# Performance work log

Measured on AMD Instinct MI355X. Metric: run time of the kernel, lower is better.

## Reference

```python
import jax, jax.numpy as jnp
import numpy as np

B, T, E, H = 2, 2048, 1024, 16
HS = E // H  # head_size = 64
EPS = 1e-5


def _layernorm(x, g, b):
    mu = jnp.mean(x, axis=-1, keepdims=True)
    var = jnp.mean(jnp.square(x - mu), axis=-1, keepdims=True)
    return (x - mu) * jax.lax.rsqrt(var + EPS) * g + b


def _block_forward(x, wq, wk, wv, wp, bp, ln1_g, ln1_b, ln2_g, ln2_b,
                   w1, b1, w2, b2, w3, b3, wg_att, bg_att, wg_ff, bg_ff):
    Bc, Tc, Ec = x.shape
    # --- multi-head causal self-attention on ln1(x) ---
    h = _layernorm(x, ln1_g, ln1_b)
    q = jnp.einsum('bte,hek->bhtk', h, wq)  # [B,H,T,HS]
    k = jnp.einsum('bte,hek->bhtk', h, wk)
    v = jnp.einsum('bte,hek->bhtk', h, wv)
    scores = jnp.einsum('bhtk,bhsk->bhts', q, k) * (HS ** -0.5)
    causal = jnp.tril(jnp.ones((Tc, Tc), dtype=bool))
    scores = jnp.where(causal, scores, jnp.finfo(scores.dtype).min)
    wei = jax.nn.softmax(scores, axis=-1)  # [B,H,T,T] (returned, as in torch)
    attn = jnp.einsum('bhts,bhsk->bhtk', wei, v)
    # concat heads in head order -> [B,T,H*HS]
    attn = attn.transpose(0, 2, 1, 3).reshape(Bc, Tc, H * HS)
    sa_out = attn @ wp + bp
    # gated residual: gate from new value, multiply residual (old x)
    gate = jax.nn.sigmoid(sa_out @ wg_att + bg_att)
    x = sa_out + gate * x
    # --- feed-forward on ln2(x) ---
    h2 = _layernorm(x, ln2_g, ln2_b)
    f = jax.nn.gelu(h2 @ w1 + b1, approximate=False)   # [B,T,4E]
    f = jax.nn.gelu(f @ w2 + b2, approximate=False)    # [B,T,2E]
    f = f @ w3 + b3                                     # [B,T,E]
    gate2 = jax.nn.sigmoid(f @ wg_ff + bg_ff)
    x = f + gate2 * x
    return x, wei


def setup_inputs() -> dict:
    key = jax.random.key(0)
    ks = jax.random.split(key, 24)
    s = 0.02
    n = lambda i, shape: (jax.random.normal(ks[i], shape) * s).astype(jnp.float32)
    return {
        'x': jax.random.normal(ks[0], (B, T, E), dtype=jnp.float32),
        'wq': n(1, (H, E, HS)), 'wk': n(2, (H, E, HS)), 'wv': n(3, (H, E, HS)),
        'wp': n(4, (H * HS, E)), 'bp': jnp.zeros((E,), jnp.float32),
        'ln1_g': jnp.ones((E,), jnp.float32), 'ln1_b': jnp.zeros((E,), jnp.float32),
        'ln2_g': jnp.ones((E,), jnp.float32), 'ln2_b': jnp.zeros((E,), jnp.float32),
        'w1': n(5, (E, 4 * E)), 'b1': jnp.zeros((4 * E,), jnp.float32),
        'w2': n(6, (4 * E, 2 * E)), 'b2': jnp.zeros((2 * E,), jnp.float32),
        'w3': n(7, (2 * E, E)), 'b3': jnp.zeros((E,), jnp.float32),
        'wg_att': n(8, (E, E)), 'bg_att': jnp.zeros((E,), jnp.float32),
        'wg_ff': n(9, (E, E)), 'bg_ff': jnp.zeros((E,), jnp.float32),
    }


def reference(x, wq, wk, wv, wp, bp, ln1_g, ln1_b, ln2_g, ln2_b,
              w1, b1, w2, b2, w3, b3, wg_att, bg_att, wg_ff, bg_ff):
    return _block_forward(x, wq, wk, wv, wp, bp, ln1_g, ln1_b, ln2_g, ln2_b,
                          w1, b1, w2, b2, w3, b3, wg_att, bg_att, wg_ff, bg_ff)
```

## Files before the change

### kernel.cpp

```cpp
#include <hip/hip_runtime.h>
#include <hip/hip_bf16.h>

typedef unsigned short u16;
typedef __attribute__((ext_vector_type(8))) short short8;
typedef __attribute__((ext_vector_type(4))) float floatx4;

#define DI __device__ __forceinline__

constexpr int Tn  = 2048;
constexpr int En  = 1024;
constexpr int BTn = 4096;

DI float bf2f(u16 u) { union { unsigned int i; float f; } v; v.i = (unsigned int)u << 16; return v.f; }
DI u16 f2bf(float f) {
  union { float f; unsigned int i; } u; u.f = f;
  unsigned int r = u.i + 0x7FFFu + ((u.i >> 16) & 1u);
  return (u16)(r >> 16);
}
DI float gelu_f(float x) { return 0.5f * x * (1.f + erff(x * 0.70710678118654752f)); }
DI float sigmoid_f(float x) { return 1.f / (1.f + __expf(-x)); }

DI void gload_lds16(const u16* g, u16* l) {
  __builtin_amdgcn_global_load_lds(
      (const __attribute__((address_space(1))) unsigned int*)g,
      (__attribute__((address_space(3))) unsigned int*)l, 16, 0, 0);
}

template <int EPI>
__launch_bounds__(256, 2)
__global__ void gemm_bt(const u16* __restrict__ A, const u16* __restrict__ Bt,
                        const float* __restrict__ bias, u16* __restrict__ C,
                        int M, int N, int K) {
  __shared__ __align__(16) u16 As[3][128 * 32];
  __shared__ __align__(16) u16 Bs[3][128 * 32];
  const int tid = threadIdx.x;
  const int m0 = blockIdx.y << 7, n0 = blockIdx.x << 7;
  const int lane = tid & 63, l15 = lane & 15, quad = lane >> 4;
  const int wave = tid >> 6;
  const int wm = (wave >> 1) << 6, wn = (wave & 1) << 6;

  const int ra = tid >> 2, c8 = (tid & 3) << 3;
  const u16* pa0 = A + (size_t)(m0 + ra) * K + c8;
  const u16* pa1 = pa0 + (size_t)64 * K;
  const u16* pb0 = Bt + (size_t)(n0 + ra) * K + c8;
  const u16* pb1 = pb0 + (size_t)64 * K;
  const int lo = ra * 32 + c8;

  auto STG = [&](int b, int kt) {
    const int ko = kt << 5;
    gload_lds16(pa0 + ko, &As[b][lo]);
    gload_lds16(pa1 + ko, &As[b][lo + 64 * 32]);
    gload_lds16(pb0 + ko, &Bs[b][lo]);
    gload_lds16(pb1 + ko, &Bs[b][lo + 64 * 32]);
  };

  const int nk = K >> 5;
  STG(0, 0); STG(1, 1); STG(2, 2);

  floatx4 acc[4][4] = {};
  int cur = 0;
  for (int k = 0; k < nk; ++k) {
    const int rem = nk - k;
    if (rem > 2)       asm volatile("s_waitcnt vmcnt(8)" ::: "memory");
    else if (rem == 2) asm volatile("s_waitcnt vmcnt(4)" ::: "memory");
    else               asm volatile("s_waitcnt vmcnt(0)" ::: "memory");
    __builtin_amdgcn_s_barrier();
    __builtin_amdgcn_sched_barrier(0);
    const u16* Ab = As[cur];
    const u16* Bb = Bs[cur];
    short8 af[4], bfr[4];
#pragma unroll
    for (int i = 0; i < 4; ++i) {
      af[i]  = *(const short8*)&Ab[(wm + i * 16 + l15) * 32 + quad * 8];
      bfr[i] = *(const short8*)&Bb[(wn + i * 16 + l15) * 32 + quad * 8];
    }
#pragma unroll
    for (int i = 0; i < 4; ++i)
#pragma unroll
      for (int j = 0; j < 4; ++j)
        acc[i][j] = __builtin_amdgcn_mfma_f32_16x16x32_bf16(af[i], bfr[j], acc[i][j], 0, 0, 0);
    __builtin_amdgcn_s_barrier();
    __builtin_amdgcn_sched_barrier(0);
    if (k + 3 < nk) STG(cur, k + 3);
    cur = (cur == 2) ? 0 : cur + 1;
  }
#pragma unroll
  for (int j = 0; j < 4; ++j) {
    const int col = n0 + wn + j * 16 + l15;
    const float bv = bias ? bias[col] : 0.f;
#pragma unroll
    for (int i = 0; i < 4; ++i) {
#pragma unroll
      for (int r = 0; r < 4; ++r) {
        const int row = m0 + wm + i * 16 + quad * 4 + r;
        float v = acc[i][j][r] + bv;
        if (EPI == 1) v = gelu_f(v);
        if (EPI == 2) v = sigmoid_f(v);
        C[(size_t)row * N + col] = f2bf(v);
      }
    }
  }
}

__launch_bounds__(256, 2)
__global__ void attn_scores(const u16* __restrict__ qkv, float* __restrict__ wei,
                            float* __restrict__ lsum) {
  const int bh = blockIdx.z, b = bh >> 4, h = bh & 15;
  const int m0 = blockIdx.y << 7, n0 = blockIdx.x << 7;
  float* weib = wei + (size_t)bh * Tn * Tn;
  const int tid = threadIdx.x;
  if (n0 > m0 + 127) {
    const float4 z = {0.f, 0.f, 0.f, 0.f};
#pragma unroll
    for (int it = 0; it < 16; ++it) {
      int lin = it * 256 + tid;
      int r = lin >> 5, c4 = (lin & 31) << 2;
      *(float4*)&weib[(size_t)(m0 + r) * Tn + n0 + c4] = z;
    }
    return;
  }
  __shared__ __align__(16) u16 Qs[128 * 64];
  __shared__ __align__(16) u16 Ks[128 * 64];
  const int lane = tid & 63, l15 = lane & 15, quad = lane >> 4;
  const int wave = tid >> 6;
  const int wm = (wave >> 1) << 6, wn = (wave & 1) << 6;
  const u16* qb = qkv + (size_t)b * Tn * 3072 + h * 64;
  const u16* kb = qb + 1024;
#pragma unroll
  for (int it = 0; it < 4; ++it) {
    int lin = it * 256 + tid;
    int r = lin >> 3, cc = (lin & 7) << 3;
    gload_lds16(&qb[(size_t)(m0 + r) * 3072 + cc], &Qs[r * 64 + cc]);
    gload_lds16(&kb[(size_t)(n0 + r) * 3072 + cc], &Ks[r * 64 + cc]);
  }
  __syncthreads();
  floatx4 acc[4][4] = {};
#pragma unroll
  for (int ks = 0; ks < 2; ++ks) {
    short8 af[4], bfr[4];
#pragma unroll
    for (int i = 0; i < 4; ++i) {
      af[i]  = *(const short8*)&Qs[(wm + i * 16 + l15) * 64 + ks * 32 + quad * 8];
      bfr[i] = *(const short8*)&Ks[(wn + i * 16 + l15) * 64 + ks * 32 + quad * 8];
    }
#pragma unroll
    for (int i = 0; i < 4; ++i)
#pragma unroll
      for (int j = 0; j < 4; ++j)
        acc[i][j] = __builtin_amdgcn_mfma_f32_16x16x32_bf16(af[i], bfr[j], acc[i][j], 0, 0, 0);
  }
#pragma unroll
  for (int i = 0; i < 4; ++i) {
#pragma unroll
    for (int r = 0; r < 4; ++r) {
      const int row = m0 + wm + i * 16 + quad * 4 + r;
      float ps = 0.f;
#pragma unroll
      for (int j = 0; j < 4; ++j) {
        const int col = n0 + wn + j * 16 + l15;
        float p = (col <= row) ? __expf(acc[i][j][r] * 0.125f) : 0.f;
        weib[(size_t)row * Tn + col] = p;
        ps += p;
      }
      float v = ps;
      v += __shfl_xor(v, 1); v += __shfl_xor(v, 2);
      v += __shfl_xor(v, 4); v += __shfl_xor(v, 8);
      if (l15 == 0) atomicAdd(&lsum[bh * Tn + row], v);
    }
  }
}

__launch_bounds__(256, 2)
__global__ void attn_pv(float* __restrict__ wei, const u16* __restrict__ vT,
                        const float* __restrict__ lsum, u16* __restrict__ attn_out) {
  const int bh = blockIdx.z, b = bh >> 4, h = bh & 15;
  const int m0 = blockIdx.x << 7;
  float* weib = wei + (size_t)bh * Tn * Tn;
  const u16* vtb = vT + (size_t)bh * 64 * Tn;
  __shared__ __align__(16) u16 Ps[128 * 32];
  __shared__ __align__(16) u16 Vs[64 * 32];
  const int tid = threadIdx.x;
  const int lane = tid & 63, l15 = lane & 15, quad = lane >> 4;
  const int wave = tid >> 6;
  const int ra = tid >> 2, c8 = (tid & 3) << 3;
  const float inv0 = 1.f / lsum[bh * Tn + m0 + ra];
  const float inv1 = 1.f / lsum[bh * Tn + m0 + ra + 64];
  floatx4 acc[2][4] = {};
  const int kmax = m0 + 128;
  for (int k0 = 0; k0 < kmax; k0 += 32) {
    gload_lds16(&vtb[(size_t)ra * Tn + k0 + c8], &Vs[ra * 32 + c8]);
#pragma unroll
    for (int half = 0; half < 2; ++half) {
      const int r = ra + half * 64;
      const float inv = half ? inv1 : inv0;
      size_t go = (size_t)(m0 + r) * Tn + k0 + c8;
      float4 a = *(float4*)&weib[go];
      float4 b4 = *(float4*)&weib[go + 4];
      a.x *= inv; a.y *= inv; a.z *= inv; a.w *= inv;
      b4.x *= inv; b4.y *= inv; b4.z *= inv; b4.w *= inv;
      u16 o8[8] = { f2bf(a.x), f2bf(a.y), f2bf(a.z), f2bf(a.w),
                    f2bf(b4.x), f2bf(b4.y), f2bf(b4.z), f2bf(b4.w) };
      *(uint4*)&Ps[r * 32 + c8] = *(uint4*)o8;
      *(float4*)&weib[go] = a;
      *(float4*)&weib[go + 4] = b4;
    }
    __syncthreads();
    short8 af[2], bfr[4];
#pragma unroll
    for (int i = 0; i < 2; ++i)
      af[i] = *(const short8*)&Ps[(wave * 32 + i * 16 + l15) * 32 + quad * 8];
#pragma unroll
    for (int j = 0; j < 4; ++j)
      bfr[j] = *(const short8*)&Vs[(j * 16 + l15) * 32 + quad * 8];
#pragma unroll
    for (int i = 0; i < 2; ++i)
#pragma unroll
      for (int j = 0; j < 4; ++j)
        acc[i][j] = __builtin_amdgcn_mfma_f32_16x16x32_bf16(af[i], bfr[j], acc[i][j], 0, 0, 0);
    __syncthreads();
  }
#pragma unroll
  for (int i = 0; i < 2; ++i)
#pragma unroll
    for (int j = 0; j < 4; ++j)
#pragma unroll
      for (int r = 0; r < 4; ++r) {
        const int row = m0 + wave * 32 + i * 16 + quad * 4 + r;
        const int col = j * 16 + l15;
        attn_out[(size_t)(b * Tn + row) * En + h * 64 + col] = f2bf(acc[i][j][r]);
      }
}

__global__ void transpose_wf(const float* __restrict__ in, u16* __restrict__ out, int R, int Cc) {
  __shared__ u16 t[64][65];
  const int tid = threadIdx.x;
  const int r0 = blockIdx.y << 6, c0 = blockIdx.x << 6;
#pragma unroll
  for (int it = 0; it < 4; ++it) {
    int lin = it * 256 + tid;
    int r = lin >> 4, c4 = (lin & 15) << 2;
    float4 v = *(const float4*)&in[(size_t)(r0 + r) * Cc + c0 + c4];
    t[r][c4 + 0] = f2bf(v.x); t[r][c4 + 1] = f2bf(v.y);
    t[r][c4 + 2] = f2bf(v.z); t[r][c4 + 3] = f2bf(v.w);
  }
  __syncthreads();
#pragma unroll
  for (int it = 0; it < 2; ++it) {
    int lin = it * 256 + tid;
    int r = lin >> 3, cc = (lin & 7) << 3;
    u16 t8[8];
#pragma unroll
    for (int e = 0; e < 8; ++e) t8[e] = t[cc + e][r];
    *(uint4*)&out[(size_t)(c0 + r) * R + r0 + cc] = *(uint4*)t8;
  }
}

__global__ void repack_qkvw(const float* __restrict__ wq, const float* __restrict__ wk,
                            const float* __restrict__ wv, u16* __restrict__ out) {
  const int which = blockIdx.z;
  const float* w = which == 0 ? wq : (which == 1 ? wk : wv);
  const int h = blockIdx.y;
  const int e0 = blockIdx.x << 6;
  __shared__ u16 t[64][65];
  const int tid = threadIdx.x;
  const float* ib = w + (size_t)h * 1024 * 64;
#pragma unroll
  for (int it = 0; it < 4; ++it) {
    int lin = it * 256 + tid;
    int r = lin >> 4, c4 = (lin & 15) << 2;
    float4 v = *(const float4*)&ib[(size_t)(e0 + r) * 64 + c4];
    t[r][c4 + 0] = f2bf(v.x); t[r][c4 + 1] = f2bf(v.y);
    t[r][c4 + 2] = f2bf(v.z); t[r][c4 + 3] = f2bf(v.w);
  }
  __syncthreads();
  u16* ob = out + ((size_t)which * 1024 + h * 64) * 1024;
#pragma unroll
  for (int it = 0; it < 2; ++it) {
    int lin = it * 256 + tid;
    int r = lin >> 3, cc = (lin & 7) << 3;
    u16 t8[8];
#pragma unroll
    for (int e = 0; e < 8; ++e) t8[e] = t[cc + e][r];
    *(uint4*)&ob[(size_t)r * 1024 + e0 + cc] = *(uint4*)t8;
  }
}

__global__ void transpose_v(const u16* __restrict__ qkv, u16* __restrict__ vT) {
  const int bh = blockIdx.z, b = bh >> 4, h = bh & 15;
  const int s0 = blockIdx.x << 6;
  __shared__ u16 t[64][65];
  const int tid = threadIdx.x;
  const u16* ib = qkv + (size_t)b * Tn * 3072 + 2048 + h * 64;
#pragma unroll
  for (int it = 0; it < 2; ++it) {
    int lin = it * 256 + tid;
    int r = lin >> 3, cc = (lin & 7) << 3;
    uint4 v = *(const uint4*)&ib[(size_t)(s0 + r) * 3072 + cc];
    u16 t8[8]; *(uint4*)t8 = v;
#pragma unroll
    for (int e = 0; e < 8; ++e) t[r][cc + e] = t8[e];
  }
  __syncthreads();
  u16* ob = vT + (size_t)bh * 64 * Tn;
#pragma unroll
  for (int it = 0; it < 2; ++it) {
    int lin = it * 256 + tid;
    int r = lin >> 3, cc = (lin & 7) << 3;
    u16 t8[8];
#pragma unroll
    for (int e = 0; e < 8; ++e) t8[e] = t[cc + e][r];
    *(uint4*)&ob[(size_t)r * Tn + s0 + cc] = *(uint4*)t8;
  }
}

__launch_bounds__(256)
__global__ void layernorm_k(const float* __restrict__ x, const float* __restrict__ g,
                            const float* __restrict__ be, u16* __restrict__ out) {
  const int row = blockIdx.x;
  const int tid = threadIdx.x;
  const float* xr = x + (size_t)row * En;
  float4 xv = *(const float4*)&xr[tid * 4];
  float s = xv.x + xv.y + xv.z + xv.w;
  float sq = xv.x * xv.x + xv.y * xv.y + xv.z * xv.z + xv.w * xv.w;
#pragma unroll
  for (int o = 1; o < 64; o <<= 1) { s += __shfl_xor(s, o); sq += __shfl_xor(sq, o); }
  __shared__ float red[8];
  const int wave = tid >> 6, lane = tid & 63;
  if (lane == 0) { red[wave] = s; red[wave + 4] = sq; }
  __syncthreads();
  const float S  = red[0] + red[1] + red[2] + red[3];
  const float SQ = red[4] + red[5] + red[6] + red[7];
  const float mu = S * (1.f / 1024.f);
  const float var = SQ * (1.f / 1024.f) - mu * mu;
  const float rstd = rsqrtf(var + 1e-5f);
  float4 gv = *(const float4*)&g[tid * 4];
  float4 bv = *(const float4*)&be[tid * 4];
  ushort4 ov;
  ov.x = f2bf((xv.x - mu) * rstd * gv.x + bv.x);
  ov.y = f2bf((xv.y - mu) * rstd * gv.y + bv.y);
  ov.z = f2bf((xv.z - mu) * rstd * gv.z + bv.z);
  ov.w = f2bf((xv.w - mu) * rstd * gv.w + bv.w);
  *(ushort4*)&out[(size_t)row * En + tid * 4] = ov;
}

__global__ void gated_residual(const u16* __restrict__ val, const u16* __restrict__ gate,
                               const float* __restrict__ res, float* __restrict__ out) {
  const size_t i = ((size_t)blockIdx.x * 256 + threadIdx.x) * 4;
  ushort4 v = *(const ushort4*)&val[i];
  ushort4 g = *(const ushort4*)&gate[i];
  float4 r = *(const float4*)&res[i];
  float4 o;
  o.x = bf2f(v.x) + bf2f(g.x) * r.x;
  o.y = bf2f(v.y) + bf2f(g.y) * r.y;
  o.z = bf2f(v.z) + bf2f(g.z) * r.z;
  o.w = bf2f(v.w) + bf2f(g.w) * r.w;
  *(float4*)&out[i] = o;
}

extern "C" void kernel_launch(void* const* d_in, const int* in_sizes, int n_in,
                              void* d_out, int out_size, void* d_ws, size_t ws_size,
                              hipStream_t stream) {
  const float* x    = (const float*)d_in[0];
  const float* wq   = (const float*)d_in[1];
  const float* wk   = (const float*)d_in[2];
  const float* wv   = (const float*)d_in[3];
  const float* wp   = (const float*)d_in[4];
  const float* bp   = (const float*)d_in[5];
  const float* ln1g = (const float*)d_in[6];
  const float* ln1b = (const float*)d_in[7];
  const float* ln2g = (const float*)d_in[8];
  const float* ln2b = (const float*)d_in[9];
  const float* w1   = (const float*)d_in[10];
  const float* b1   = (const float*)d_in[11];
  const float* w2   = (const float*)d_in[12];
  const float* b2   = (const float*)d_in[13];
  const float* w3   = (const float*)d_in[14];
  const float* b3   = (const float*)d_in[15];
  const float* wga  = (const float*)d_in[16];
  const float* bga  = (const float*)d_in[17];
  const float* wgf  = (const float*)d_in[18];
  const float* bgf  = (const float*)d_in[19];

  float* out_x = (float*)d_out;
  float* wei   = out_x + (size_t)BTn * En;

  char* wsb = (char*)d_ws;
  size_t off = 0;
  auto alloc = [&](size_t bytes) { char* p = wsb + off; off += (bytes + 255) & ~(size_t)255; return p; };
  float* lsum = (float*)alloc((size_t)32 * Tn * 4);
  u16* WqkvT = (u16*)alloc((size_t)3072 * 1024 * 2);
  u16* wpT   = (u16*)alloc((size_t)1024 * 1024 * 2);
  u16* wgaT  = (u16*)alloc((size_t)1024 * 1024 * 2);
  u16* w1T   = (u16*)alloc((size_t)4096 * 1024 * 2);
  u16* w2T   = (u16*)alloc((size_t)2048 * 4096 * 2);
  u16* w3T   = (u16*)alloc((size_t)1024 * 2048 * 2);
  u16* wgfT  = (u16*)alloc((size_t)1024 * 1024 * 2);
  u16* h1    = (u16*)alloc((size_t)BTn * En * 2);
  u16* qkv   = (u16*)alloc((size_t)BTn * 3072 * 2);
  u16* vT    = (u16*)alloc((size_t)32 * 64 * Tn * 2);
  u16* attn  = (u16*)alloc((size_t)BTn * En * 2);
  u16* sa    = (u16*)alloc((size_t)BTn * En * 2);
  u16* glin  = (u16*)alloc((size_t)BTn * En * 2);
  float* x1  = (float*)alloc((size_t)BTn * En * 4);
  u16* h2 = h1;
  u16* f1 = qkv;
  u16* f2 = attn;
  u16* f3 = glin;
  u16* g2 = h1;

  hipMemsetAsync(lsum, 0, (size_t)32 * Tn * 4, stream);
  repack_qkvw<<<dim3(16, 16, 3), 256, 0, stream>>>(wq, wk, wv, WqkvT);
  transpose_wf<<<dim3(16, 16), 256, 0, stream>>>(wp,  wpT,  1024, 1024);
  transpose_wf<<<dim3(16, 16), 256, 0, stream>>>(wga, wgaT, 1024, 1024);
  transpose_wf<<<dim3(64, 16), 256, 0, stream>>>(w1,  w1T,  1024, 4096);
  transpose_wf<<<dim3(32, 64), 256, 0, stream>>>(w2,  w2T,  4096, 2048);
  transpose_wf<<<dim3(16, 32), 256, 0, stream>>>(w3,  w3T,  2048, 1024);
  transpose_wf<<<dim3(16, 16), 256, 0, stream>>>(wgf, wgfT, 1024, 1024);

  layernorm_k<<<BTn, 256, 0, stream>>>(x, ln1g, ln1b, h1);
  gemm_bt<0><<<dim3(24, 32), 256, 0, stream>>>(h1, WqkvT, nullptr, qkv, BTn, 3072, 1024);
  transpose_v<<<dim3(32, 1, 32), 256, 0, stream>>>(qkv, vT);
  attn_scores<<<dim3(16, 16, 32), 256, 0, stream>>>(qkv, wei, lsum);
  attn_pv<<<dim3(16, 1, 32), 256, 0, stream>>>(wei, vT, lsum, attn);
  gemm_bt<0><<<dim3(8, 32), 256, 0, stream>>>(attn, wpT, bp, sa, BTn, 1024, 1024);
  gemm_bt<2><<<dim3(8, 32), 256, 0, stream>>>(sa, wgaT, bga, glin, BTn, 1024, 1024);
  gated_residual<<<BTn, 256, 0, stream>>>(sa, glin, x, x1);
  layernorm_k<<<BTn, 256, 0, stream>>>(x1, ln2g, ln2b, h2);
  gemm_bt<1><<<dim3(32, 32), 256, 0, stream>>>(h2, w1T, b1, f1, BTn, 4096, 1024);
  gemm_bt<1><<<dim3(16, 32), 256, 0, stream>>>(f1, w2T, b2, f2, BTn, 2048, 4096);
  gemm_bt<0><<<dim3(8, 32), 256, 0, stream>>>(f2, w3T, b3, f3, BTn, 1024, 2048);
  gemm_bt<2><<<dim3(8, 32), 256, 0, stream>>>(f3, wgfT, bgf, g2, BTn, 1024, 1024);
  gated_residual<<<BTn, 256, 0, stream>>>(f3, g2, x1, out_x);
}
```

Baseline: 1.304 ms.

## Fuse attention probs and PV into one kernel, recompute QK instead of rereading wei

The scores kernel now only computes row sums of exp(scores), plus zero-fills the upper triangle; it no longer writes the lower triangle of wei. A new fused kernel recomputes QK^T per tile, normalizes by the row sum, writes the final fp32 probabilities once and feeds bf16 P into the PV MFMA. K and V tiles are double-buffered in swizzled LDS, and row tiles are ordered to balance causal work. This removes one fp32 write plus a read-modify-write of the large wei tensor, at the cost of computing QK^T twice and a more complex pipeline.

```diff
diff --git a/kernel.cpp b/kernel.cpp
--- a/kernel.cpp
+++ b/kernel.cpp
@@ -103,7 +103,7 @@
 }
 
 __launch_bounds__(256, 2)
-__global__ void attn_scores(const u16* __restrict__ qkv, float* __restrict__ wei,
+__global__ void attn_rowsum(const u16* __restrict__ qkv, float* __restrict__ wei,
                             float* __restrict__ lsum) {
   const int bh = blockIdx.z, b = bh >> 4, h = bh & 15;
   const int m0 = blockIdx.y << 7, n0 = blockIdx.x << 7;
@@ -130,8 +130,9 @@
   for (int it = 0; it < 4; ++it) {
     int lin = it * 256 + tid;
     int r = lin >> 3, cc = (lin & 7) << 3;
-    gload_lds16(&qb[(size_t)(m0 + r) * 3072 + cc], &Qs[r * 64 + cc]);
-    gload_lds16(&kb[(size_t)(n0 + r) * 3072 + cc], &Ks[r * 64 + cc]);
+    int cs = cc ^ ((r & 7) << 3);
+    gload_lds16(&qb[(size_t)(m0 + r) * 3072 + cs], &Qs[r * 64 + cc]);
+    gload_lds16(&kb[(size_t)(n0 + r) * 3072 + cs], &Ks[r * 64 + cc]);
   }
   __syncthreads();
   floatx4 acc[4][4] = {};
@@ -140,8 +141,10 @@
     short8 af[4], bfr[4];
 #pragma unroll
     for (int i = 0; i < 4; ++i) {
-      af[i]  = *(const short8*)&Qs[(wm + i * 16 + l15) * 64 + ks * 32 + quad * 8];
-      bfr[i] = *(const short8*)&Ks[(wn + i * 16 + l15) * 64 + ks * 32 + quad * 8];
+      const int qr = wm + i * 16 + l15;
+      const int kr = wn + i * 16 + l15;
+      af[i]  = *(const short8*)&Qs[qr * 64 + ((ks * 32 + quad * 8) ^ ((qr & 7) << 3))];
+      bfr[i] = *(const short8*)&Ks[kr * 64 + ((ks * 32 + quad * 8) ^ ((kr & 7) << 3))];
     }
 #pragma unroll
     for (int i = 0; i < 4; ++i)
@@ -159,7 +162,6 @@
       for (int j = 0; j < 4; ++j) {
         const int col = n0 + wn + j * 16 + l15;
         float p = (col <= row) ? __expf(acc[i][j][r] * 0.125f) : 0.f;
-        weib[(size_t)row * Tn + col] = p;
         ps += p;
       }
       float v = ps;
@@ -170,64 +172,149 @@
   }
 }
 
-__launch_bounds__(256, 2)
-__global__ void attn_pv(float* __restrict__ wei, const u16* __restrict__ vT,
-                        const float* __restrict__ lsum, u16* __restrict__ attn_out) {
+__launch_bounds__(512, 2)
+__global__ void attn_fused(const u16* __restrict__ qkv, const u16* __restrict__ vT,
+                           const float* __restrict__ lsum, float* __restrict__ wei,
+                           u16* __restrict__ attn_out) {
   const int bh = blockIdx.z, b = bh >> 4, h = bh & 15;
-  const int m0 = blockIdx.x << 7;
+  const int xm = blockIdx.x;
+  const int mt = (xm & 1) ? (15 - (xm >> 1)) : (xm >> 1);
+  const int m0 = mt << 7;
   float* weib = wei + (size_t)bh * Tn * Tn;
+  const u16* qb = qkv + (size_t)b * Tn * 3072 + h * 64;
+  const u16* kb = qb + 1024;
   const u16* vtb = vT + (size_t)bh * 64 * Tn;
-  __shared__ __align__(16) u16 Ps[128 * 32];
-  __shared__ __align__(16) u16 Vs[64 * 32];
+
+  __shared__ __align__(16) u16 Ks[2][128 * 64];
+  __shared__ __align__(16) u16 Vs[2][64 * 128];
+  __shared__ __align__(16) u16 Ps[128 * 128];
+
   const int tid = threadIdx.x;
   const int lane = tid & 63, l15 = lane & 15, quad = lane >> 4;
-  const int wave = tid >> 6;
-  const int ra = tid >> 2, c8 = (tid & 3) << 3;
-  const float inv0 = 1.f / lsum[bh * Tn + m0 + ra];
-  const float inv1 = 1.f / lsum[bh * Tn + m0 + ra + 64];
-  floatx4 acc[2][4] = {};
-  const int kmax = m0 + 128;
-  for (int k0 = 0; k0 < kmax; k0 += 32) {
-    gload_lds16(&vtb[(size_t)ra * Tn + k0 + c8], &Vs[ra * 32 + c8]);
-#pragma unroll
-    for (int half = 0; half < 2; ++half) {
-      const int r = ra + half * 64;
-      const float inv = half ? inv1 : inv0;
-      size_t go = (size_t)(m0 + r) * Tn + k0 + c8;
-      float4 a = *(float4*)&weib[go];
-      float4 b4 = *(float4*)&weib[go + 4];
-      a.x *= inv; a.y *= inv; a.z *= inv; a.w *= inv;
-      b4.x *= inv; b4.y *= inv; b4.z *= inv; b4.w *= inv;
-      u16 o8[8] = { f2bf(a.x), f2bf(a.y), f2bf(a.z), f2bf(a.w),
-                    f2bf(b4.x), f2bf(b4.y), f2bf(b4.z), f2bf(b4.w) };
-      *(uint4*)&Ps[r * 32 + c8] = *(uint4*)o8;
-      *(float4*)&weib[go] = a;
-      *(float4*)&weib[go + 4] = b4;
-    }
-    __syncthreads();
-    short8 af[2], bfr[4];
-#pragma unroll
-    for (int i = 0; i < 2; ++i)
-      af[i] = *(const short8*)&Ps[(wave * 32 + i * 16 + l15) * 32 + quad * 8];
-#pragma unroll
-    for (int j = 0; j < 4; ++j)
-      bfr[j] = *(const short8*)&Vs[(j * 16 + l15) * 32 + quad * 8];
-#pragma unroll
-    for (int i = 0; i < 2; ++i)
-#pragma unroll
-      for (int j = 0; j < 4; ++j)
-        acc[i][j] = __builtin_amdgcn_mfma_f32_16x16x32_bf16(af[i], bfr[j], acc[i][j], 0, 0, 0);
-    __syncthreads();
-  }
-#pragma unroll
-  for (int i = 0; i < 2; ++i)
-#pragma unroll
-    for (int j = 0; j < 4; ++j)
+  const int w = tid >> 6;
+  const int rm = w >> 2, cn = w & 3;
+  const int pm = w >> 1, pc = w & 1;
+
+  const int rk = tid >> 3, ck = (tid & 7) << 3;
+  const int rv = tid >> 4, cv = (tid & 15) << 3;
+  const int cks = ck ^ ((rk & 7) << 3);
+  const int cvs = cv ^ ((rv & 7) << 3);
+
+  auto STAGE = [&](int buf, int nt) {
+    const int n0 = nt << 7;
+    gload_lds16(&kb[(size_t)(n0 + rk) * 3072 + cks], &Ks[buf][rk * 64 + ck]);
+    gload_lds16(&kb[(size_t)(n0 + 64 + rk) * 3072 + cks], &Ks[buf][(64 + rk) * 64 + ck]);
+    gload_lds16(&vtb[(size_t)rv * Tn + n0 + cvs], &Vs[buf][rv * 128 + cv]);
+    gload_lds16(&vtb[(size_t)(32 + rv) * Tn + n0 + cvs], &Vs[buf][(32 + rv) * 128 + cv]);
+  };
+
+  gload_lds16(&qb[(size_t)(m0 + rk) * 3072 + cks], &Ps[rk * 64 + ck]);
+  gload_lds16(&qb[(size_t)(m0 + 64 + rk) * 3072 + cks], &Ps[(64 + rk) * 64 + ck]);
+  STAGE(0, 0);
+  if (mt >= 1) {
+    STAGE(1, 1);
+    asm volatile("s_waitcnt vmcnt(8)" ::: "memory");
+  } else {
+    asm volatile("s_waitcnt vmcnt(4)" ::: "memory");
+  }
+  __builtin_amdgcn_s_barrier();
+  __builtin_amdgcn_sched_barrier(0);
+
+  short8 af[4][2];
+#pragma unroll
+  for (int i = 0; i < 4; ++i)
+#pragma unroll
+    for (int ks = 0; ks < 2; ++ks) {
+      const int qr = rm * 64 + i * 16 + l15;
+      af[i][ks] = *(const short8*)&Ps[qr * 64 + ((ks * 32 + quad * 8) ^ ((qr & 7) << 3))];
+    }
+  asm volatile("s_waitcnt lgkmcnt(0)" ::: "memory");
+  __builtin_amdgcn_sched_barrier(0);
+  __builtin_amdgcn_s_barrier();
+  __builtin_amdgcn_sched_barrier(0);
+
+  float inv[4][4];
+#pragma unroll
+  for (int i = 0; i < 4; ++i)
+#pragma unroll
+    for (int r = 0; r < 4; ++r)
+      inv[i][r] = 1.f / lsum[bh * Tn + m0 + rm * 64 + i * 16 + quad * 4 + r];
+
+  floatx4 acc_o[2][2] = {};
+  for (int nt = 0; nt <= mt; ++nt) {
+    const int cbuf = nt & 1;
+    if (nt < mt) asm volatile("s_waitcnt vmcnt(4)" ::: "memory");
+    else         asm volatile("s_waitcnt vmcnt(0)" ::: "memory");
+    __builtin_amdgcn_s_barrier();
+    __builtin_amdgcn_sched_barrier(0);
+
+    floatx4 acc_s[4][2] = {};
+#pragma unroll
+    for (int ks = 0; ks < 2; ++ks) {
+      short8 bk[2];
+#pragma unroll
+      for (int j = 0; j < 2; ++j) {
+        const int kr = cn * 32 + j * 16 + l15;
+        bk[j] = *(const short8*)&Ks[cbuf][kr * 64 + ((ks * 32 + quad * 8) ^ ((kr & 7) << 3))];
+      }
+#pragma unroll
+      for (int i = 0; i < 4; ++i)
+#pragma unroll
+        for (int j = 0; j < 2; ++j)
+          acc_s[i][j] = __builtin_amdgcn_mfma_f32_16x16x32_bf16(af[i][ks], bk[j], acc_s[i][j], 0, 0, 0);
+    }
+
+    const int n0 = nt << 7;
+#pragma unroll
+    for (int i = 0; i < 4; ++i)
+#pragma unroll
+      for (int j = 0; j < 2; ++j)
+#pragma unroll
+        for (int r = 0; r < 4; ++r) {
+          const int prow = rm * 64 + i * 16 + quad * 4 + r;
+          const int pcol = cn * 32 + j * 16 + l15;
+          const int row = m0 + prow, col = n0 + pcol;
+          float p = (col <= row) ? __expf(acc_s[i][j][r] * 0.125f) * inv[i][r] : 0.f;
+          weib[(size_t)row * Tn + col] = p;
+          Ps[prow * 128 + (pcol ^ ((prow & 7) << 3))] = f2bf(p);
+        }
+    asm volatile("s_waitcnt lgkmcnt(0)" ::: "memory");
+    __builtin_amdgcn_s_barrier();
+    __builtin_amdgcn_sched_barrier(0);
+
+#pragma unroll
+    for (int k = 0; k < 4; ++k) {
+      short8 pa[2], vb[2];
+#pragma unroll
+      for (int i2 = 0; i2 < 2; ++i2) {
+        const int pr = pm * 32 + i2 * 16 + l15;
+        pa[i2] = *(const short8*)&Ps[pr * 128 + ((k * 32 + quad * 8) ^ ((pr & 7) << 3))];
+      }
+#pragma unroll
+      for (int j2 = 0; j2 < 2; ++j2) {
+        const int vr = pc * 32 + j2 * 16 + l15;
+        vb[j2] = *(const short8*)&Vs[cbuf][vr * 128 + ((k * 32 + quad * 8) ^ ((vr & 7) << 3))];
+      }
+#pragma unroll
+      for (int i2 = 0; i2 < 2; ++i2)
+#pragma unroll
+        for (int j2 = 0; j2 < 2; ++j2)
+          acc_o[i2][j2] = __builtin_amdgcn_mfma_f32_16x16x32_bf16(pa[i2], vb[j2], acc_o[i2][j2], 0, 0, 0);
+    }
+    __builtin_amdgcn_s_barrier();
+    __builtin_amdgcn_sched_barrier(0);
+    if (nt + 2 <= mt) STAGE(cbuf, nt + 2);
+  }
+
+#pragma unroll
+  for (int i2 = 0; i2 < 2; ++i2)
+#pragma unroll
+    for (int j2 = 0; j2 < 2; ++j2)
 #pragma unroll
       for (int r = 0; r < 4; ++r) {
-        const int row = m0 + wave * 32 + i * 16 + quad * 4 + r;
-        const int col = j * 16 + l15;
-        attn_out[(size_t)(b * Tn + row) * En + h * 64 + col] = f2bf(acc[i][j][r]);
+        const int row = m0 + pm * 32 + i2 * 16 + quad * 4 + r;
+        const int col = pc * 32 + j2 * 16 + l15;
+        attn_out[(size_t)(b * Tn + row) * En + h * 64 + col] = f2bf(acc_o[i2][j2][r]);
       }
 }
 
@@ -420,8 +507,8 @@
   layernorm_k<<<BTn, 256, 0, stream>>>(x, ln1g, ln1b, h1);
   gemm_bt<0><<<dim3(24, 32), 256, 0, stream>>>(h1, WqkvT, nullptr, qkv, BTn, 3072, 1024);
   transpose_v<<<dim3(32, 1, 32), 256, 0, stream>>>(qkv, vT);
-  attn_scores<<<dim3(16, 16, 32), 256, 0, stream>>>(qkv, wei, lsum);
-  attn_pv<<<dim3(16, 1, 32), 256, 0, stream>>>(wei, vT, lsum, attn);
+  attn_rowsum<<<dim3(16, 16, 32), 256, 0, stream>>>(qkv, wei, lsum);
+  attn_fused<<<dim3(16, 1, 32), 512, 0, stream>>>(qkv, vT, lsum, wei, attn);
   gemm_bt<0><<<dim3(8, 32), 256, 0, stream>>>(attn, wpT, bp, sa, BTn, 1024, 1024);
   gemm_bt<2><<<dim3(8, 32), 256, 0, stream>>>(sa, wgaT, bga, glin, BTn, 1024, 1024);
   gated_residual<<<BTn, 256, 0, stream>>>(sa, glin, x, x1);
```

Result: faster. 1.126 ms (-13.7%).
